# Kernel tuning notes

Measured on AMD Instinct MI355X. Metric: run time of the kernel, lower is better.

Reference implementation:

```python
import jax, jax.numpy as jnp
import numpy as np

D = 256  # in_channels == out_channels -> output_proj is Identity


def setup_inputs() -> dict:
    key = jax.random.key(0)
    ks = jax.random.split(key, 7)
    B, N = 4, 4096
    s = 1.0 / np.sqrt(D)
    return {
        "x": jax.random.normal(ks[0], (B, N, D), dtype=jnp.float32),
        "Wk": jax.random.normal(ks[1], (D, D), dtype=jnp.float32) * s,
        "bk": jax.random.normal(ks[2], (D,), dtype=jnp.float32) * 0.01,
        "Wq": jax.random.normal(ks[3], (D, D), dtype=jnp.float32) * s,
        "bq": jax.random.normal(ks[4], (D,), dtype=jnp.float32) * 0.01,
        "Wv": jax.random.normal(ks[5], (D, D), dtype=jnp.float32) * s,
        "bv": jax.random.normal(ks[6], (D,), dtype=jnp.float32) * 0.01,
    }


def reference(x, Wk, bk, Wq, bq, Wv, bv):
    # Linear projections: torch Linear(x) = x @ W.T + b; here W is stored as [in, out]
    keys = jnp.einsum("bnd,de->bne", x, Wk) + bk
    queries = jnp.einsum("bnd,de->bne", x, Wq) + bq
    values = jnp.einsum("bnd,de->bne", x, Wv) + bv
    scale = 1.0 / jnp.sqrt(jnp.float32(D))
    scores = jnp.einsum("bqd,bkd->bqk", queries, keys) * scale  # [B, N, N]
    attn = jax.nn.softmax(scores, axis=-1)
    out = jnp.einsum("bqk,bkd->bqd", attn, values)
    return out
```

## Files before the change

kernel.cpp:

```cpp
#include <hip/hip_runtime.h>
#include <hip/hip_bf16.h>


typedef __attribute__((ext_vector_type(8))) short bf16x8;
typedef __attribute__((ext_vector_type(4))) float f32x4;

__device__ __forceinline__ float b2f(ushort u){
  union { uint i; float f; } v; v.i = ((uint)u) << 16; return v.f;
}
__device__ __forceinline__ ushort f2b(float f){
  union { float f; uint i; } v; v.f = f;
  uint i = v.i;
  return (ushort)((i + 0x7FFFu + ((i >> 16) & 1u)) >> 16);
}
__device__ __forceinline__ uint pack2(float a, float b){
  return (uint)f2b(a) | ((uint)f2b(b) << 16);
}
__device__ __forceinline__ uint fbits(float f){
  union { float f; uint i; } v; v.f = f; return v.i;
}

__device__ __forceinline__ void gl_lds16(const ushort* g, ushort* l){
  __builtin_amdgcn_global_load_lds(
      (const __attribute__((address_space(1))) uint*)g,
      (__attribute__((address_space(3))) uint*)l, 16, 0, 0);
}

#define Q_SCALE 0.0901684400555602f
#define FIXED_M 16.0f

__global__ __launch_bounds__(256) void transpose_w_kernel(
    const float* __restrict__ Wk, const float* __restrict__ Wq,
    const float* __restrict__ Wv, ushort* __restrict__ Wt){
  __shared__ ushort t[64][72];
  const float* src = (blockIdx.y == 0) ? Wk : (blockIdx.y == 1) ? Wq : Wv;
  ushort* dst = Wt + blockIdx.y * 65536;
  int tile = blockIdx.x;
  int tr = tile >> 2, tc = tile & 3;
  int tid = threadIdx.x;
  for (int i = tid; i < 1024; i += 256){
    int r = i >> 4, ch = i & 15;
    float4 f = *(const float4*)(src + (tr*64 + r)*256 + tc*64 + ch*4);
    uint2 u; u.x = pack2(f.x, f.y); u.y = pack2(f.z, f.w);
    *(uint2*)&t[r][ch*4] = u;
  }
  __syncthreads();
  for (int i = tid; i < 2048; i += 256){
    int c = i >> 5, r2 = (i & 31)*2;
    uint v = (uint)t[r2][c] | ((uint)t[r2+1][c] << 16);
    *(uint*)(dst + (tc*64 + c)*256 + tr*64 + r2) = v;
  }
}

__global__ __launch_bounds__(256) void proj_kernel(
    const float* __restrict__ x, const ushort* __restrict__ Wt,
    const float* __restrict__ bK, const float* __restrict__ bQ,
    const float* __restrict__ bV,
    ushort* __restrict__ Ko, ushort* __restrict__ Qo, ushort* __restrict__ Vt){
  __shared__ ushort xs[64][264];
  __shared__ ushort wt[2][16][264];
  int my = blockIdx.y;
  int n0 = blockIdx.x * 64;
  const ushort* wsrc = Wt + my*65536;
  const float* bias  = (my==0) ? bK : (my==1) ? bQ : bV;

  int tid = threadIdx.x;
  int lane = tid & 63, w = tid >> 6, quad = lane >> 4, l16 = lane & 15;

  for (int i = tid; i < 4096; i += 256){
    int r = i >> 6, ch = i & 63;
    float4 f = *(const float4*)(x + (size_t)(n0 + r)*256 + ch*4);
    uint2 u; u.x = pack2(f.x, f.y); u.y = pack2(f.z, f.w);
    *(uint2*)&xs[r][ch*4] = u;
  }

  int seg0 = tid*2,     r0 = seg0 >> 5, c0 = seg0 & 31;
  int seg1 = tid*2 + 1, r1 = seg1 >> 5, c1 = seg1 & 31;
  {
    uint4 a = *(const uint4*)(wsrc + r0*256 + c0*8);
    uint4 b = *(const uint4*)(wsrc + r1*256 + c1*8);
    *(uint4*)&wt[0][r0][c0*8] = a;
    *(uint4*)&wt[0][r1][c1*8] = b;
  }
  __syncthreads();

  bf16x8 afr[8];
  #pragma unroll
  for (int ks = 0; ks < 8; ks++)
    afr[ks] = *(const bf16x8*)&xs[w*16 + l16][ks*32 + quad*8];

  for (int nt = 0; nt < 16; nt++){
    int cu = nt & 1;
    uint4 wa, wb;
    if (nt < 15){
      const ushort* wn = wsrc + (nt+1)*4096;
      wa = *(const uint4*)(wn + r0*256 + c0*8);
      wb = *(const uint4*)(wn + r1*256 + c1*8);
    }
    f32x4 acc = {0.f, 0.f, 0.f, 0.f};
    #pragma unroll
    for (int ks = 0; ks < 8; ks++){
      bf16x8 bfr = *(const bf16x8*)&wt[cu][l16][ks*32 + quad*8];
      acc = __builtin_amdgcn_mfma_f32_16x16x32_bf16(afr[ks], bfr, acc, 0, 0, 0);
    }
    int e = nt*16 + l16;
    float bv = bias[e];
    if (my == 2){
      int b  = n0 >> 12;
      int nl = (n0 & 4095) + w*16 + quad*4;
      ushort* vb = Vt + (size_t)b*1048576 + (size_t)e*4096 + nl;
      #pragma unroll
      for (int r = 0; r < 4; r++) vb[r] = f2b(acc[r] + bv);
    } else {
      float scale = (my==1) ? Q_SCALE : 1.0f;
      ushort* out = (my==0) ? Ko : Qo;
      #pragma unroll
      for (int r = 0; r < 4; r++){
        int row = n0 + w*16 + quad*4 + r;
        out[(size_t)row*256 + e] = f2b((acc[r] + bv) * scale);
      }
    }
    if (nt < 15){
      *(uint4*)&wt[cu^1][r0][c0*8] = wa;
      *(uint4*)&wt[cu^1][r1][c1*8] = wb;
    }
    __syncthreads();
  }
}

__global__ __launch_bounds__(256, 2) void attn_kernel(
    const ushort* __restrict__ Q, const ushort* __restrict__ K,
    const ushort* __restrict__ Vt,
    float* __restrict__ O0, ushort* __restrict__ Obf, float* __restrict__ lp){
  __shared__ ushort Kbuf[2][8192];
  __shared__ ushort Vbuf[2][8192];
  __shared__ ushort Ps[128][40];

  int bx   = blockIdx.x;
  int bh   = bx & 15;
  int b    = bh >> 2;
  int half = bh & 3;
  int qt   = bx >> 4;
  int tid = threadIdx.x, lane = tid & 63, w = tid >> 6;
  int quad = lane >> 4, l16 = lane & 15;

  const ushort* Qb = Q  + (size_t)(b*4096 + qt*128)*256;
  const ushort* Kb = K  + (size_t)b*4096*256;
  const ushort* Vb = Vt + (size_t)b*256*4096;

  int kOff[4], vOff[4];
  #pragma unroll
  for (int i = 0; i < 4; i++){
    int off16 = (w*4 + i)*64 + lane;
    int krow = off16 >> 5, ks_ = off16 & 31;
    int g    = ks_ ^ (krow & 7);
    kOff[i]  = krow*256 + g*8;
    int sr = off16 >> 3, sl = off16 & 7;
    int xv = sl ^ (sr & 7);
    int d  = sr*2 + ((xv >> 2) & 1), c = xv & 3;
    vOff[i] = d*4096 + c*8;
  }
  int m7 = l16 & 7;
  int kslot[8];
  #pragma unroll
  for (int ks = 0; ks < 8; ks++) kslot[ks] = ((ks*4 + quad) ^ m7) * 8;
  int vlane = (((l16 >> 1)*8) + (((l16 & 1)*4 + quad) ^ (l16 >> 1))) * 8;

  bf16x8 qf[2][8];
  #pragma unroll
  for (int s = 0; s < 2; s++)
    #pragma unroll
    for (int ks = 0; ks < 8; ks++)
      qf[s][ks] = *(const bf16x8*)(Qb + (size_t)(w*32 + s*16 + l16)*256 + ks*32 + quad*8);

  f32x4 of[2][16];
  #pragma unroll
  for (int s = 0; s < 2; s++)
    #pragma unroll
    for (int dt = 0; dt < 16; dt++) of[s][dt] = (f32x4){0.f, 0.f, 0.f, 0.f};
  float l_i[2][4];
  #pragma unroll
  for (int s = 0; s < 2; s++)
    #pragma unroll
    for (int r = 0; r < 4; r++) l_i[s][r] = 0.f;

  int kt0 = half * 32, kt1 = kt0 + 32;

  #pragma unroll
  for (int i = 0; i < 4; i++){
    gl_lds16(Kb + (size_t)kt0*8192 + kOff[i], &Kbuf[0][(w*4 + i)*512]);
    gl_lds16(Vb + (size_t)kt0*32   + vOff[i], &Vbuf[0][(w*4 + i)*512]);
  }
  __syncthreads();

  int cur = 0;
  for (int kt = kt0; kt < kt1; kt++){
    int nxt = cur ^ 1;
    if (kt + 1 < kt1){
      #pragma unroll
      for (int i = 0; i < 4; i++){
        gl_lds16(Kb + (size_t)(kt+1)*8192 + kOff[i], &Kbuf[nxt][(w*4 + i)*512]);
        gl_lds16(Vb + (size_t)(kt+1)*32   + vOff[i], &Vbuf[nxt][(w*4 + i)*512]);
      }
    }
    const ushort* Kc = &Kbuf[cur][0];
    const ushort* Vc = &Vbuf[cur][0];

    f32x4 sf[2][2];
    #pragma unroll
    for (int s = 0; s < 2; s++)
      #pragma unroll
      for (int nt = 0; nt < 2; nt++) sf[s][nt] = (f32x4){0.f, 0.f, 0.f, 0.f};
    #pragma unroll
    for (int nt = 0; nt < 2; nt++){
      const ushort* Kr = Kc + nt*4096 + l16*256;
      #pragma unroll
      for (int ks = 0; ks < 8; ks++){
        bf16x8 bfr = *(const bf16x8*)(Kr + kslot[ks]);
        sf[0][nt] = __builtin_amdgcn_mfma_f32_16x16x32_bf16(qf[0][ks], bfr, sf[0][nt], 0,0,0);
        sf[1][nt] = __builtin_amdgcn_mfma_f32_16x16x32_bf16(qf[1][ks], bfr, sf[1][nt], 0,0,0);
      }
    }

    #pragma unroll
    for (int s = 0; s < 2; s++){
      #pragma unroll
      for (int r = 0; r < 4; r++){
        float p0 = exp2f(sf[s][0][r] - FIXED_M);
        float p1 = exp2f(sf[s][1][r] - FIXED_M);
        l_i[s][r] += p0 + p1;
        uint pb = __builtin_amdgcn_perm(fbits(p1) + 0x8000u,
                                        fbits(p0) + 0x8000u, 0x07060302u);
        ushort* prow = &Ps[w*32 + s*16 + quad*4 + r][0];
        prow[l16]      = (ushort)pb;
        prow[16 + l16] = (ushort)(pb >> 16);
      }
    }

    bf16x8 pf0 = *(const bf16x8*)&Ps[w*32 +      l16][quad*8];
    bf16x8 pf1 = *(const bf16x8*)&Ps[w*32 + 16 + l16][quad*8];
    #pragma unroll
    for (int dt = 0; dt < 16; dt++){
      bf16x8 vf = *(const bf16x8*)(Vc + dt*512 + vlane);
      of[0][dt] = __builtin_amdgcn_mfma_f32_16x16x32_bf16(pf0, vf, of[0][dt], 0, 0, 0);
      of[1][dt] = __builtin_amdgcn_mfma_f32_16x16x32_bf16(pf1, vf, of[1][dt], 0, 0, 0);
    }

    __syncthreads();
    cur = nxt;
  }

  #pragma unroll
  for (int s = 0; s < 2; s++)
    #pragma unroll
    for (int r = 0; r < 4; r++){
      float rs = l_i[s][r];
      #pragma unroll
      for (int msk = 1; msk < 16; msk <<= 1) rs += __shfl_xor(rs, msk, 16);
      l_i[s][r] = rs;
    }

  #pragma unroll
  for (int s = 0; s < 2; s++){
    int gq0 = b*4096 + qt*128 + w*32 + s*16 + quad*4;
    if (l16 == 0){
      #pragma unroll
      for (int r = 0; r < 4; r++)
        lp[(size_t)half*16384 + gq0 + r] = l_i[s][r];
    }
    if (half == 0){
      #pragma unroll
      for (int dt = 0; dt < 16; dt++)
        #pragma unroll
        for (int r = 0; r < 4; r++)
          O0[(size_t)(gq0 + r)*256 + dt*16 + l16] = of[s][dt][r];
    } else {
      ushort* Oh = Obf + (size_t)(half - 1)*16384*256;
      #pragma unroll
      for (int dt = 0; dt < 16; dt++)
        #pragma unroll
        for (int r = 0; r < 4; r++)
          Oh[(size_t)(gq0 + r)*256 + dt*16 + l16] = f2b(of[s][dt][r]);
    }
  }
}

__global__ __launch_bounds__(256) void merge_kernel(
    float* __restrict__ O0, const ushort* __restrict__ Obf,
    const float* __restrict__ lp){
  int t   = blockIdx.x*256 + threadIdx.x;
  int row = t >> 6;
  int c   = (t & 63) * 4;
  float den = lp[row] + lp[16384 + row] + lp[2*16384 + row] + lp[3*16384 + row];
  float rden = 1.0f / den;
  size_t idx = (size_t)row*256 + c;
  float4 acc = *(float4*)&O0[idx];
  #pragma unroll
  for (int h = 1; h < 4; h++){
    ushort4 oh = *(const ushort4*)&Obf[(size_t)(h-1)*16384*256 + idx];
    acc.x += b2f(oh.x); acc.y += b2f(oh.y);
    acc.z += b2f(oh.z); acc.w += b2f(oh.w);
  }
  acc.x *= rden; acc.y *= rden; acc.z *= rden; acc.w *= rden;
  *(float4*)&O0[idx] = acc;
}

extern "C" void kernel_launch(void* const* d_in, const int* in_sizes, int n_in,
                              void* d_out, int out_size, void* d_ws, size_t ws_size,
                              hipStream_t stream){
  const float* x  = (const float*)d_in[0];
  const float* Wk = (const float*)d_in[1];
  const float* bk = (const float*)d_in[2];
  const float* Wq = (const float*)d_in[3];
  const float* bq = (const float*)d_in[4];
  const float* Wv = (const float*)d_in[5];
  const float* bv = (const float*)d_in[6];

  char* ws = (char*)d_ws;
  ushort* Wt  = (ushort*)(ws);
  ushort* Qb  = (ushort*)(ws + (size_t)1*(1u<<20));
  ushort* Kb  = (ushort*)(ws + (size_t)10*(1u<<20));
  ushort* Vtb = (ushort*)(ws + (size_t)19*(1u<<20));
  ushort* Obf = (ushort*)(ws + (size_t)28*(1u<<20));
  float*  lp  = (float*)(ws + (size_t)54*(1u<<20));

  hipLaunchKernelGGL(transpose_w_kernel, dim3(16, 3), dim3(256), 0, stream,
                     Wk, Wq, Wv, Wt);
  hipLaunchKernelGGL(proj_kernel, dim3(256, 3), dim3(256), 0, stream,
                     x, Wt, bk, bq, bv, Kb, Qb, Vtb);
  hipLaunchKernelGGL(attn_kernel, dim3(512), dim3(256), 0, stream,
                     Qb, Kb, Vtb, (float*)d_out, Obf, lp);
  hipLaunchKernelGGL(merge_kernel, dim3(4096), dim3(256), 0, stream,
                     (float*)d_out, Obf, lp);
}
```

Baseline: 203.3 us.

## Fuse split-KV merge into attention via last-block atomic counter; single-pass projection

The standalone merge kernel is removed. Each attention block now writes its partial output as bf16 and increments a per-tile atomic counter, and the last of the four KV-split blocks does the normalization and sum into the output. The projection kernel now computes all three projections in one block per row tile, so x is loaded and converted once instead of three times. The cost is less projection parallelism (256 blocks instead of 768) and a serialized merge tail in the last attention block. Half 0's partial is also stored as bf16 now rather than fp32.

```diff
diff --git a/kernel.cpp b/kernel.cpp
--- a/kernel.cpp
+++ b/kernel.cpp
@@ -31,8 +31,11 @@
 
 __global__ __launch_bounds__(256) void transpose_w_kernel(
     const float* __restrict__ Wk, const float* __restrict__ Wq,
-    const float* __restrict__ Wv, ushort* __restrict__ Wt){
+    const float* __restrict__ Wv, ushort* __restrict__ Wt,
+    int* __restrict__ cnt){
   __shared__ ushort t[64][72];
+  if (blockIdx.x == 0 && blockIdx.y == 0 && threadIdx.x < 128)
+    cnt[threadIdx.x] = 0;
   const float* src = (blockIdx.y == 0) ? Wk : (blockIdx.y == 1) ? Wq : Wv;
   ushort* dst = Wt + blockIdx.y * 65536;
   int tile = blockIdx.x;
@@ -59,10 +62,7 @@
     ushort* __restrict__ Ko, ushort* __restrict__ Qo, ushort* __restrict__ Vt){
   __shared__ ushort xs[64][264];
   __shared__ ushort wt[2][16][264];
-  int my = blockIdx.y;
   int n0 = blockIdx.x * 64;
-  const ushort* wsrc = Wt + my*65536;
-  const float* bias  = (my==0) ? bK : (my==1) ? bQ : bV;
 
   int tid = threadIdx.x;
   int lane = tid & 63, w = tid >> 6, quad = lane >> 4, l16 = lane & 15;
@@ -77,8 +77,8 @@
   int seg0 = tid*2,     r0 = seg0 >> 5, c0 = seg0 & 31;
   int seg1 = tid*2 + 1, r1 = seg1 >> 5, c1 = seg1 & 31;
   {
-    uint4 a = *(const uint4*)(wsrc + r0*256 + c0*8);
-    uint4 b = *(const uint4*)(wsrc + r1*256 + c1*8);
+    uint4 a = *(const uint4*)(Wt + r0*256 + c0*8);
+    uint4 b = *(const uint4*)(Wt + r1*256 + c1*8);
     *(uint4*)&wt[0][r0][c0*8] = a;
     *(uint4*)&wt[0][r1][c1*8] = b;
   }
@@ -89,11 +89,12 @@
   for (int ks = 0; ks < 8; ks++)
     afr[ks] = *(const bf16x8*)&xs[w*16 + l16][ks*32 + quad*8];
 
-  for (int nt = 0; nt < 16; nt++){
-    int cu = nt & 1;
+  for (int it = 0; it < 48; it++){
+    int my = it >> 4, nt = it & 15;
+    int cu = it & 1;
     uint4 wa, wb;
-    if (nt < 15){
-      const ushort* wn = wsrc + (nt+1)*4096;
+    if (it < 47){
+      const ushort* wn = Wt + (it+1)*4096;
       wa = *(const uint4*)(wn + r0*256 + c0*8);
       wb = *(const uint4*)(wn + r1*256 + c1*8);
     }
@@ -104,6 +105,7 @@
       acc = __builtin_amdgcn_mfma_f32_16x16x32_bf16(afr[ks], bfr, acc, 0, 0, 0);
     }
     int e = nt*16 + l16;
+    const float* bias = (my==0) ? bK : (my==1) ? bQ : bV;
     float bv = bias[e];
     if (my == 2){
       int b  = n0 >> 12;
@@ -120,7 +122,7 @@
         out[(size_t)row*256 + e] = f2b((acc[r] + bv) * scale);
       }
     }
-    if (nt < 15){
+    if (it < 47){
       *(uint4*)&wt[cu^1][r0][c0*8] = wa;
       *(uint4*)&wt[cu^1][r1][c1*8] = wb;
     }
@@ -131,10 +133,12 @@
 __global__ __launch_bounds__(256, 2) void attn_kernel(
     const ushort* __restrict__ Q, const ushort* __restrict__ K,
     const ushort* __restrict__ Vt,
-    float* __restrict__ O0, ushort* __restrict__ Obf, float* __restrict__ lp){
+    float* __restrict__ out, ushort* __restrict__ Obf,
+    float* __restrict__ lp, int* __restrict__ cnt){
   __shared__ ushort Kbuf[2][8192];
   __shared__ ushort Vbuf[2][8192];
   __shared__ ushort Ps[128][40];
+  __shared__ int s_last;
 
   int bx   = blockIdx.x;
   int bh   = bx & 15;
@@ -260,6 +264,7 @@
       l_i[s][r] = rs;
     }
 
+  ushort* Oh = Obf + (size_t)half*16384*256;
   #pragma unroll
   for (int s = 0; s < 2; s++){
     int gq0 = b*4096 + qt*128 + w*32 + s*16 + quad*4;
@@ -268,41 +273,37 @@
       for (int r = 0; r < 4; r++)
         lp[(size_t)half*16384 + gq0 + r] = l_i[s][r];
     }
-    if (half == 0){
-      #pragma unroll
-      for (int dt = 0; dt < 16; dt++)
-        #pragma unroll
-        for (int r = 0; r < 4; r++)
-          O0[(size_t)(gq0 + r)*256 + dt*16 + l16] = of[s][dt][r];
-    } else {
-      ushort* Oh = Obf + (size_t)(half - 1)*16384*256;
-      #pragma unroll
-      for (int dt = 0; dt < 16; dt++)
-        #pragma unroll
-        for (int r = 0; r < 4; r++)
-          Oh[(size_t)(gq0 + r)*256 + dt*16 + l16] = f2b(of[s][dt][r]);
-    }
-  }
-}
-
-__global__ __launch_bounds__(256) void merge_kernel(
-    float* __restrict__ O0, const ushort* __restrict__ Obf,
-    const float* __restrict__ lp){
-  int t   = blockIdx.x*256 + threadIdx.x;
-  int row = t >> 6;
-  int c   = (t & 63) * 4;
-  float den = lp[row] + lp[16384 + row] + lp[2*16384 + row] + lp[3*16384 + row];
-  float rden = 1.0f / den;
-  size_t idx = (size_t)row*256 + c;
-  float4 acc = *(float4*)&O0[idx];
-  #pragma unroll
-  for (int h = 1; h < 4; h++){
-    ushort4 oh = *(const ushort4*)&Obf[(size_t)(h-1)*16384*256 + idx];
-    acc.x += b2f(oh.x); acc.y += b2f(oh.y);
-    acc.z += b2f(oh.z); acc.w += b2f(oh.w);
-  }
-  acc.x *= rden; acc.y *= rden; acc.z *= rden; acc.w *= rden;
-  *(float4*)&O0[idx] = acc;
+    #pragma unroll
+    for (int dt = 0; dt < 16; dt++)
+      #pragma unroll
+      for (int r = 0; r < 4; r++)
+        Oh[(size_t)(gq0 + r)*256 + dt*16 + l16] = f2b(of[s][dt][r]);
+  }
+
+  __threadfence();
+  __syncthreads();
+  if (tid == 0) s_last = (atomicAdd(&cnt[b*32 + qt], 1) == 3);
+  __syncthreads();
+  if (s_last){
+    __threadfence();
+    int base = b*4096 + qt*128;
+    for (int i = tid; i < 8192; i += 256){
+      int row = i >> 6, c = (i & 63)*4;
+      float den = lp[base + row] + lp[16384 + base + row]
+                + lp[2*16384 + base + row] + lp[3*16384 + base + row];
+      float rden = 1.0f / den;
+      size_t idx = (size_t)(base + row)*256 + c;
+      float4 acc = {0.f, 0.f, 0.f, 0.f};
+      #pragma unroll
+      for (int h = 0; h < 4; h++){
+        ushort4 oh = *(const ushort4*)&Obf[(size_t)h*16384*256 + idx];
+        acc.x += b2f(oh.x); acc.y += b2f(oh.y);
+        acc.z += b2f(oh.z); acc.w += b2f(oh.w);
+      }
+      acc.x *= rden; acc.y *= rden; acc.z *= rden; acc.w *= rden;
+      *(float4*)&out[idx] = acc;
+    }
+  }
 }
 
 extern "C" void kernel_launch(void* const* d_in, const int* in_sizes, int n_in,
@@ -322,14 +323,13 @@
   ushort* Kb  = (ushort*)(ws + (size_t)10*(1u<<20));
   ushort* Vtb = (ushort*)(ws + (size_t)19*(1u<<20));
   ushort* Obf = (ushort*)(ws + (size_t)28*(1u<<20));
-  float*  lp  = (float*)(ws + (size_t)54*(1u<<20));
+  float*  lp  = (float*)(ws + (size_t)62*(1u<<20));
+  int*    cnt = (int*)(ws + (size_t)63*(1u<<20));
 
   hipLaunchKernelGGL(transpose_w_kernel, dim3(16, 3), dim3(256), 0, stream,
-                     Wk, Wq, Wv, Wt);
-  hipLaunchKernelGGL(proj_kernel, dim3(256, 3), dim3(256), 0, stream,
+                     Wk, Wq, Wv, Wt, cnt);
+  hipLaunchKernelGGL(proj_kernel, dim3(256), dim3(256), 0, stream,
                      x, Wt, bk, bq, bv, Kb, Qb, Vtb);
   hipLaunchKernelGGL(attn_kernel, dim3(512), dim3(256), 0, stream,
-                     Qb, Kb, Vtb, (float*)d_out, Obf, lp);
-  hipLaunchKernelGGL(merge_kernel, dim3(4096), dim3(256), 0, stream,
-                     (float*)d_out, Obf, lp);
-}
+                     Qb, Kb, Vtb, (float*)d_out, Obf, lp, cnt);
+}
```

Result: slower. 358.6 us (+76.4%).
